# Kernel tuning notes

Hardware: AMD Instinct MI355X
Metric: run time of the kernel (lower is better)

Reference implementation:

```python
import jax, jax.numpy as jnp
import numpy as np
from jax import lax

B, S, HDIM = 4, 2048, 1024
H, D, L = 16, 64, 128
NB = S // L
EPS = 1e-8


def setup_inputs() -> dict:
    key = jax.random.key(0)
    ks = jax.random.split(key, 16)
    std = 0.02
    inp = {
        'f_in': jax.random.normal(ks[0], (B, S, HDIM), jnp.float32),
        'i_in': jax.random.normal(ks[1], (B, S, HDIM), jnp.float32),
        'z_in': jax.random.normal(ks[2], (B, S, HDIM), jnp.float32),
        'o_in': jax.random.normal(ks[3], (B, S, HDIM), jnp.float32),
        'c0': jax.random.normal(ks[4], (B, H, D), jnp.float32),
        'h0': jax.random.normal(ks[5], (B, H, D), jnp.float32),
        # weights stored (in, out) so forward is x @ W + b
        'Wf': std * jax.random.normal(ks[6], (HDIM, H * D), jnp.float32),
        'bf': jnp.zeros((H * D,), jnp.float32),
        'Wi': std * jax.random.normal(ks[7], (HDIM, H * D), jnp.float32),
        'bi': jnp.zeros((H * D,), jnp.float32),
        'Wz': std * jax.random.normal(ks[8], (HDIM, H * D), jnp.float32),
        'bz': jnp.zeros((H * D,), jnp.float32),
        'Wo': std * jax.random.normal(ks[9], (HDIM, H * D), jnp.float32),
        'bo': jnp.zeros((H * D,), jnp.float32),
        'Wp': std * jax.random.normal(ks[10], (H * D, HDIM), jnp.float32),
        'bp': jnp.zeros((HDIM,), jnp.float32),
    }
    return inp


def _to_blocks(x):
    # (B,S,H*D) -> (NB, B, H, D, L), matching torch view+permute(1,0,3,4,2)
    return jnp.transpose(x.reshape(B, NB, L, H, D), (1, 0, 3, 4, 2))


def _qlstm(f_in, i_in, z_in, o_in, c0, Wf, bf, Wi, bi, Wz, bz, Wo, bo, Wp, bp):
    fx = _to_blocks(f_in @ Wf + bf)
    ix = _to_blocks(i_in @ Wi + bi)
    zx = _to_blocks(z_in @ Wz + bz)
    ox = _to_blocks(o_in @ Wo + bo)

    f = jax.nn.sigmoid(fx + 1.0)              # (NB,B,H,D,L)
    o = jax.nn.sigmoid(ox)
    update = jax.nn.sigmoid(ix) * jnp.tanh(zx)

    kk = jnp.arange(L)[:, None]
    ll = jnp.arange(L + 1)[None, :]
    ones_mask = ll >= kk + 1                   # (L, L+1): filled with 1.0
    zeros_mask = ll >= kk + 2                  # (L, L+1): zeroed out

    def block_step(c, blk):
        fb, ob, ub = blk                       # each (B,H,D,L)
        cf = jnp.concatenate([fb, jnp.ones(fb.shape[:-1] + (1,), fb.dtype)], axis=-1)  # (B,H,D,L+1)
        Fm = jnp.broadcast_to(cf[..., None, :], fb.shape[:-1] + (L, L + 1))
        Fm = jnp.where(ones_mask, 1.0, Fm)
        # reversed log-cumsum-exp along last axis (decay products)
        Fm = jnp.exp(jnp.flip(jnp.cumsum(jnp.flip(jnp.log(Fm + EPS), -1), -1), -1)) - EPS
        Fm = jnp.where(zeros_mask, 0.0, Fm)    # (B,H,D,L,L+1)
        u = jnp.concatenate([c[..., None], ub], axis=-1)   # (B,H,D,L+1)
        cs = jnp.einsum('bhdkl,bhdl->bhdk', Fm, u)          # (B,H,D,L)
        hs = ob * jnp.tanh(cs)
        return cs[..., -1], hs

    last_c, hs = lax.scan(block_step, c0, (f, o, update))   # hs: (NB,B,H,D,L)
    last_h = hs[-1, ..., -1]
    y = jnp.transpose(hs, (1, 0, 4, 2, 3)).reshape(B, S, H * D)
    y = y @ Wp + bp                            # (B,S,HDIM)
    return y, last_c, last_h


def reference(f_in, i_in, z_in, o_in, c0, h0, Wf, bf, Wi, bi, Wz, bz, Wo, bo, Wp, bp):
    y, last_c, last_h = _qlstm(f_in, i_in, z_in, o_in, c0,
                               Wf, bf, Wi, bi, Wz, bz, Wo, bo, Wp, bp)
    return y, last_c, last_h
```

## Files before the change

kernel.cpp:

```cpp
#include <hip/hip_runtime.h>
#include <hip/hip_bf16.h>
#include <stdint.h>

constexpr int GM = 8192;
constexpr int GK = 1024;
constexpr int GN = 1024;
constexpr size_t NACT = (size_t)GM * GN;
constexpr int CHUNK = 32;
constexpr int NCHUNK = 64;
constexpr int NCH = 4096;
constexpr int NT = GK / 64;

#define DEVINL __device__ __forceinline__

typedef __attribute__((ext_vector_type(8))) short bf16x8;
typedef __attribute__((ext_vector_type(4))) float f32x4;

DEVINL float sigmoidf_(float x) { return 1.0f / (1.0f + __expf(-x)); }

DEVINL unsigned short f2bf(float x) {
  unsigned int u = __builtin_bit_cast(unsigned int, x);
  unsigned int rnd = 0x7fffu + ((u >> 16) & 1u);
  return (unsigned short)((u + rnd) >> 16);
}
DEVINL float bf2f(unsigned short u) {
  unsigned int x = ((unsigned int)u) << 16;
  return __builtin_bit_cast(float, x);
}

DEVINL void gload16(const void* g, void* l) {
  __builtin_amdgcn_global_load_lds(
      (const __attribute__((address_space(1))) unsigned int*)g,
      (__attribute__((address_space(3))) unsigned int*)l, 16, 0, 0);
}

#define SB() __builtin_amdgcn_sched_barrier(0)

struct PrepArgs {
  const float* csrc[4];
  unsigned short* cdst[4];
  const float* tsrc[5];
  unsigned short* tdst[5];
};

__global__ __launch_bounds__(256) void prep_kernel(PrepArgs p) {
  const int bx = blockIdx.x;
  if (bx < 4096) {
    const float* s = p.csrc[bx >> 10];
    unsigned short* d = p.cdst[bx >> 10];
    int i = (bx & 1023) * 256 + threadIdx.x;
    const int stride = 1024 * 256;
#pragma unroll
    for (int it = 0; it < 8; ++it, i += stride) {
      float4 v = ((const float4*)s)[i];
      ushort4 o;
      o.x = f2bf(v.x); o.y = f2bf(v.y); o.z = f2bf(v.z); o.w = f2bf(v.w);
      ((ushort4*)d)[i] = o;
    }
  } else {
    const int t = bx - 4096;
    const float* __restrict__ W = p.tsrc[t >> 10];
    unsigned short* __restrict__ Wt = p.tdst[t >> 10];
    const int rem = t & 1023;
    const int n0 = (rem & 31) * 32, k0 = (rem >> 5) * 32;
    __shared__ float tile[32][33];
    int tx = threadIdx.x & 31, ty = threadIdx.x >> 5;
#pragma unroll
    for (int i = 0; i < 32; i += 8)
      tile[ty + i][tx] = W[(size_t)(k0 + ty + i) * GN + n0 + tx];
    __syncthreads();
#pragma unroll
    for (int i = 0; i < 32; i += 8)
      Wt[(size_t)(n0 + ty + i) * GK + k0 + tx] = f2bf(tile[tx][ty + i]);
  }
}

DEVINL void gemm256_core(const unsigned short* __restrict__ A,
                         const unsigned short* __restrict__ W,
                         char* lds, int tid, int wave, int lane,
                         int bm, int bn, f32x4 (&acc)[8][4]) {
  const int Ah = wave >> 2;
  const int wn = (wave & 3) * 64;
  const int lrow = lane & 15;
  const int lgrp = lane >> 4;

  const char* gsrc[8];
  char* ldst[8];
  {
    const char* Ag = (const char*)A;
    const char* Wg = (const char*)W;
#pragma unroll
    for (int hh = 0; hh < 4; ++hh)
#pragma unroll
      for (int j = 0; j < 2; ++j) {
        const int lbyte = j * 8192 + tid * 16;
        const int row = lbyte >> 7;
        const int gcb = (lbyte & 127) ^ ((row & 7) << 4);
        const int i = hh * 2 + j;
        gsrc[i] = (hh < 2)
            ? Ag + (size_t)(bm * 256 + hh * 128 + row) * 2048 + gcb
            : Wg + (size_t)(bn * 256 + (hh - 2) * 128 + row) * 2048 + gcb;
        ldst[i] = lds + (hh >= 2 ? 32768 : 0) + (hh & 1) * 16384 + j * 8192 +
                  wave * 1024;
      }
  }

#pragma unroll
  for (int i = 0; i < 8; ++i) gload16(gsrc[i], ldst[i]);

  bf16x8 aF[4][2], bF[4][2];

  for (int t = 0; t < NT; ++t) {
    const int cur = t & 1;
    const int obuf = (cur ^ 1) * 65536;
    const char* Abase = lds + cur * 65536 + Ah * 16384;
    const char* Bbase = lds + cur * 65536 + 32768;
    const int nk = (t + 1 < NT) ? (t + 1) : (NT - 1);
    const size_t koff = (size_t)nk * 128;

#pragma unroll
    for (int i = 0; i < 4; ++i) gload16(gsrc[i] + koff, ldst[i] + obuf);
    asm volatile("s_waitcnt vmcnt(4)" ::: "memory");
    __builtin_amdgcn_s_barrier();
    SB();
#pragma unroll
    for (int m = 0; m < 4; ++m)
#pragma unroll
      for (int ks = 0; ks < 2; ++ks) {
        const int r = m * 16 + lrow;
        const int cb = ks * 64 + lgrp * 16;
        aF[m][ks] = *(const bf16x8*)(Abase + r * 128 + (cb ^ ((r & 7) << 4)));
      }
#pragma unroll
    for (int n = 0; n < 2; ++n)
#pragma unroll
      for (int ks = 0; ks < 2; ++ks) {
        const int nr = wn + n * 16 + lrow;
        const int cb = ks * 64 + lgrp * 16;
        bF[n][ks] = *(const bf16x8*)(Bbase + nr * 128 + (cb ^ ((nr & 7) << 4)));
      }
    __builtin_amdgcn_s_setprio(1);
#pragma unroll
    for (int m = 0; m < 4; ++m)
#pragma unroll
      for (int n = 0; n < 2; ++n)
#pragma unroll
        for (int ks = 0; ks < 2; ++ks)
          acc[m][n] = __builtin_amdgcn_mfma_f32_16x16x32_bf16(aF[m][ks], bF[n][ks],
                                                              acc[m][n], 0, 0, 0);
    __builtin_amdgcn_s_setprio(0);

#pragma unroll
    for (int n = 2; n < 4; ++n)
#pragma unroll
      for (int ks = 0; ks < 2; ++ks) {
        const int nr = wn + n * 16 + lrow;
        const int cb = ks * 64 + lgrp * 16;
        bF[n][ks] = *(const bf16x8*)(Bbase + nr * 128 + (cb ^ ((nr & 7) << 4)));
      }
#pragma unroll
    for (int i = 4; i < 8; ++i) gload16(gsrc[i] + koff, ldst[i] + obuf);
    __builtin_amdgcn_s_barrier();
    asm volatile("s_waitcnt lgkmcnt(0)" ::: "memory");
    SB();
    __builtin_amdgcn_s_setprio(1);
#pragma unroll
    for (int m = 0; m < 4; ++m)
#pragma unroll
      for (int n = 2; n < 4; ++n)
#pragma unroll
        for (int ks = 0; ks < 2; ++ks)
          acc[m][n] = __builtin_amdgcn_mfma_f32_16x16x32_bf16(aF[m][ks], bF[n][ks],
                                                              acc[m][n], 0, 0, 0);
    __builtin_amdgcn_s_setprio(0);

#pragma unroll
    for (int m = 0; m < 4; ++m)
#pragma unroll
      for (int ks = 0; ks < 2; ++ks) {
        const int r = (m + 4) * 16 + lrow;
        const int cb = ks * 64 + lgrp * 16;
        aF[m][ks] = *(const bf16x8*)(Abase + r * 128 + (cb ^ ((r & 7) << 4)));
      }
    __builtin_amdgcn_s_barrier();
    asm volatile("s_waitcnt lgkmcnt(0)" ::: "memory");
    SB();
    __builtin_amdgcn_s_setprio(1);
#pragma unroll
    for (int m = 0; m < 4; ++m)
#pragma unroll
      for (int n = 2; n < 4; ++n)
#pragma unroll
        for (int ks = 0; ks < 2; ++ks)
          acc[m + 4][n] = __builtin_amdgcn_mfma_f32_16x16x32_bf16(aF[m][ks], bF[n][ks],
                                                                  acc[m + 4][n], 0, 0, 0);
    __builtin_amdgcn_s_setprio(0);

    __builtin_amdgcn_s_setprio(1);
#pragma unroll
    for (int m = 0; m < 4; ++m)
#pragma unroll
      for (int n = 0; n < 2; ++n)
#pragma unroll
        for (int ks = 0; ks < 2; ++ks)
          acc[m + 4][n] = __builtin_amdgcn_mfma_f32_16x16x32_bf16(aF[m][ks], bF[n][ks],
                                                                  acc[m + 4][n], 0, 0, 0);
    __builtin_amdgcn_s_setprio(0);
  }
}

struct GateArgs {
  const unsigned short* A[4];
  const unsigned short* W[4];
  const float* bias[4];
  unsigned short* out[4];
};

__global__ __launch_bounds__(512, 2) void gemm_gates8(GateArgs ga) {
  extern __shared__ char lds[];
  const int tid = threadIdx.x;
  const int wave = tid >> 6, lane = tid & 63;
  const int bm = blockIdx.x, bn = blockIdx.y, gz = blockIdx.z;
  const int wm = (wave >> 2) * 128, wn = (wave & 3) * 64;
  const int lrow = lane & 15, lgrp = lane >> 4;

  f32x4 acc[8][4];
#pragma unroll
  for (int m = 0; m < 8; ++m)
#pragma unroll
    for (int n = 0; n < 4; ++n) acc[m][n] = (f32x4){0.f, 0.f, 0.f, 0.f};

  gemm256_core(ga.A[gz], ga.W[gz], lds, tid, wave, lane, bm, bn, acc);

  const float* bias = ga.bias[gz];
  unsigned short* out = ga.out[gz];
  float bv[4];
#pragma unroll
  for (int n = 0; n < 4; ++n) bv[n] = bias[bn * 256 + wn + n * 16 + lrow];

#pragma unroll
  for (int m = 0; m < 8; ++m)
#pragma unroll
    for (int n = 0; n < 4; ++n) {
      const int gc = bn * 256 + wn + n * 16 + lrow;
#pragma unroll
      for (int j = 0; j < 4; ++j) {
        const int gr = bm * 256 + wm + m * 16 + lgrp * 4 + j;
        float v = acc[m][n][j] + bv[n];
        if (gz == 0) v = sigmoidf_(v + 1.0f);
        else if (gz == 1) v = sigmoidf_(v);
        out[(size_t)gr * GN + gc] = f2bf(v);
      }
    }
}

__global__ __launch_bounds__(512, 2) void gemm_proj_bn128(
    const unsigned short* __restrict__ A, const unsigned short* __restrict__ W,
    const float* __restrict__ bias, float* __restrict__ out) {
  extern __shared__ char lds[];
  const int tid = threadIdx.x;
  const int wave = tid >> 6, lane = tid & 63;
  const int bm = blockIdx.x, bn = blockIdx.y;
  const int wm = (wave >> 2) * 128, wn = (wave & 3) * 32;
  const int lrow = lane & 15, lgrp = lane >> 4;

  f32x4 acc[8][2];
#pragma unroll
  for (int m = 0; m < 8; ++m)
#pragma unroll
    for (int n = 0; n < 2; ++n) acc[m][n] = (f32x4){0.f, 0.f, 0.f, 0.f};

  const char* gsrc[6];
  char* ldst[6];
  {
    const char* Ag = (const char*)A;
    const char* Wg = (const char*)W;
#pragma unroll
    for (int i = 0; i < 4; ++i) {
      const int lbyte = i * 8192 + tid * 16;
      const int row = lbyte >> 7;
      const int gcb = (lbyte & 127) ^ ((row & 7) << 4);
      gsrc[i] = Ag + (size_t)(bm * 256 + row) * 2048 + gcb;
      ldst[i] = lds + i * 8192 + wave * 1024;
    }
#pragma unroll
    for (int j = 0; j < 2; ++j) {
      const int lbyte = j * 8192 + tid * 16;
      const int row = lbyte >> 7;
      const int gcb = (lbyte & 127) ^ ((row & 7) << 4);
      gsrc[4 + j] = Wg + (size_t)(bn * 128 + row) * 2048 + gcb;
      ldst[4 + j] = lds + 65536 + j * 8192 + wave * 1024;
    }
  }

#pragma unroll
  for (int i = 0; i < 6; ++i) gload16(gsrc[i], ldst[i]);

  bf16x8 aLo[4][2], aHi[4][2], bF[2][2];

  for (int t = 0; t < NT; ++t) {
    const int cur = t & 1;
    const int obufA = (cur ^ 1) * 32768;
    const int obufB = (cur ^ 1) * 16384;
    const char* Abase = lds + cur * 32768;
    const char* Bbase = lds + 65536 + cur * 16384;
    const int nk = (t + 1 < NT) ? (t + 1) : (NT - 1);
    const size_t koff = (size_t)nk * 128;

#pragma unroll
    for (int i = 0; i < 4; ++i) gload16(gsrc[i] + koff, ldst[i] + obufA);
    asm volatile("s_waitcnt vmcnt(4)" ::: "memory");
    __builtin_amdgcn_s_barrier();
    SB();
#pragma unroll
    for (int m = 0; m < 4; ++m)
#pragma unroll
      for (int ks = 0; ks < 2; ++ks) {
        const int r = wm + m * 16 + lrow;
        const int cb = ks * 64 + lgrp * 16;
        aLo[m][ks] = *(const bf16x8*)(Abase + r * 128 + (cb ^ ((r & 7) << 4)));
      }
#pragma unroll
    for (int n = 0; n < 2; ++n)
#pragma unroll
      for (int ks = 0; ks < 2; ++ks) {
        const int nr = wn + n * 16 + lrow;
        const int cb = ks * 64 + lgrp * 16;
        bF[n][ks] = *(const bf16x8*)(Bbase + nr * 128 + (cb ^ ((nr & 7) << 4)));
      }
    __builtin_amdgcn_s_setprio(1);
#pragma unroll
    for (int m = 0; m < 4; ++m)
#pragma unroll
      for (int n = 0; n < 2; ++n)
#pragma unroll
        for (int ks = 0; ks < 2; ++ks)
          acc[m][n] = __builtin_amdgcn_mfma_f32_16x16x32_bf16(aLo[m][ks], bF[n][ks],
                                                              acc[m][n], 0, 0, 0);
    __builtin_amdgcn_s_setprio(0);

#pragma unroll
    for (int m = 0; m < 4; ++m)
#pragma unroll
      for (int ks = 0; ks < 2; ++ks) {
        const int r = wm + (m + 4) * 16 + lrow;
        const int cb = ks * 64 + lgrp * 16;
        aHi[m][ks] = *(const bf16x8*)(Abase + r * 128 + (cb ^ ((r & 7) << 4)));
      }
#pragma unroll
    for (int j = 4; j < 6; ++j) gload16(gsrc[j] + koff, ldst[j] + obufB);
    __builtin_amdgcn_s_barrier();
    asm volatile("s_waitcnt lgkmcnt(0)" ::: "memory");
    SB();
    __builtin_amdgcn_s_setprio(1);
#pragma unroll
    for (int m = 0; m < 4; ++m)
#pragma unroll
      for (int n = 0; n < 2; ++n)
#pragma unroll
        for (int ks = 0; ks < 2; ++ks)
          acc[m + 4][n] = __builtin_amdgcn_mfma_f32_16x16x32_bf16(aHi[m][ks], bF[n][ks],
                                                                  acc[m + 4][n], 0, 0, 0);
    __builtin_amdgcn_s_setprio(0);
  }

  float bv[2];
#pragma unroll
  for (int n = 0; n < 2; ++n) bv[n] = bias[bn * 128 + wn + n * 16 + lrow];

#pragma unroll
  for (int m = 0; m < 8; ++m)
#pragma unroll
    for (int n = 0; n < 2; ++n) {
      const int gc = bn * 128 + wn + n * 16 + lrow;
#pragma unroll
      for (int j = 0; j < 4; ++j) {
        const int gr = bm * 256 + wm + m * 16 + lgrp * 4 + j;
        out[(size_t)gr * GN + gc] = acc[m][n][j] + bv[n];
      }
    }
}

__global__ void scan_phaseA_kernel(const unsigned short* __restrict__ F,
                                   const unsigned short* __restrict__ Ip,
                                   const unsigned short* __restrict__ Zp,
                                   float* __restrict__ Pt, float* __restrict__ Ct) {
  int tid = blockIdx.x * blockDim.x + threadIdx.x;
  int ch = tid & (NCH - 1), chunk = tid >> 12;
  int b = ch >> 10, n = ch & 1023;
  size_t base = ((size_t)(b * 2048 + chunk * CHUNK)) * 1024 + n;
  float c = 0.f, P = 1.f;
#pragma unroll 8
  for (int t = 0; t < CHUNK; ++t) {
    size_t idx = base + (size_t)t * 1024;
    float f = bf2f(F[idx]);
    float u = sigmoidf_(bf2f(Ip[idx])) * tanhf(bf2f(Zp[idx]));
    c = __builtin_fmaf(f, c, u);
    P *= f;
  }
  Pt[tid] = P;
  Ct[tid] = c;
}

__global__ void scan_combine_kernel(const float* __restrict__ Pt,
                                    const float* __restrict__ Ct,
                                    const float* __restrict__ c0,
                                    float* __restrict__ Cin,
                                    float* __restrict__ last_c) {
  int ch = blockIdx.x * blockDim.x + threadIdx.x;
  float c = c0[ch];
#pragma unroll
  for (int j = 0; j < NCHUNK; ++j) {
    Cin[j * NCH + ch] = c;
    c = __builtin_fmaf(Pt[j * NCH + ch], c, Ct[j * NCH + ch]);
  }
  last_c[ch] = c;
}

__global__ void scan_phaseC_kernel(const unsigned short* __restrict__ F,
                                   const unsigned short* __restrict__ Ip,
                                   const unsigned short* __restrict__ Zp,
                                   const unsigned short* __restrict__ O,
                                   const float* __restrict__ Cin,
                                   unsigned short* __restrict__ Hb,
                                   float* __restrict__ last_h) {
  int tid = blockIdx.x * blockDim.x + threadIdx.x;
  int ch = tid & (NCH - 1), chunk = tid >> 12;
  int b = ch >> 10, n = ch & 1023;
  size_t base = ((size_t)(b * 2048 + chunk * CHUNK)) * 1024 + n;
  float c = Cin[tid];
  float h = 0.f;
#pragma unroll 8
  for (int t = 0; t < CHUNK; ++t) {
    size_t idx = base + (size_t)t * 1024;
    float f = bf2f(F[idx]);
    float u = sigmoidf_(bf2f(Ip[idx])) * tanhf(bf2f(Zp[idx]));
    float o = bf2f(O[idx]);
    c = __builtin_fmaf(f, c, u);
    h = o * tanhf(c);
    Hb[idx] = f2bf(h);
  }
  if (chunk == NCHUNK - 1) last_h[ch] = h;
}

extern "C" void kernel_launch(void* const* d_in, const int* in_sizes, int n_in,
                              void* d_out, int out_size, void* d_ws, size_t ws_size,
                              hipStream_t stream) {
  const float* f_in = (const float*)d_in[0];
  const float* i_in = (const float*)d_in[1];
  const float* z_in = (const float*)d_in[2];
  const float* o_in = (const float*)d_in[3];
  const float* c0 = (const float*)d_in[4];
  const float* Wf = (const float*)d_in[6];
  const float* bf_ = (const float*)d_in[7];
  const float* Wi = (const float*)d_in[8];
  const float* bi = (const float*)d_in[9];
  const float* Wz = (const float*)d_in[10];
  const float* bz = (const float*)d_in[11];
  const float* Wo = (const float*)d_in[12];
  const float* bo = (const float*)d_in[13];
  const float* Wp = (const float*)d_in[14];
  const float* bp = (const float*)d_in[15];

  float* y = (float*)d_out;
  float* last_c = y + NACT;
  float* last_h = last_c + NCH;

  char* w = (char*)d_ws;
  const size_t ABYTES = NACT * 2;
  const size_t WBYTES = (size_t)GK * GN * 2;
  unsigned short* Af = (unsigned short*)(w + 0 * ABYTES);
  unsigned short* Ai = (unsigned short*)(w + 1 * ABYTES);
  unsigned short* Az = (unsigned short*)(w + 2 * ABYTES);
  unsigned short* Ao = (unsigned short*)(w + 3 * ABYTES);
  char* wt = w + 4 * ABYTES;
  unsigned short* Wtf = (unsigned short*)(wt + 0 * WBYTES);
  unsigned short* Wti = (unsigned short*)(wt + 1 * WBYTES);
  unsigned short* Wtz = (unsigned short*)(wt + 2 * WBYTES);
  unsigned short* Wto = (unsigned short*)(wt + 3 * WBYTES);
  unsigned short* Wtp = (unsigned short*)(wt + 4 * WBYTES);
  char* gp = wt + 5 * WBYTES;
  unsigned short* F = (unsigned short*)(gp + 0 * ABYTES);
  unsigned short* O = (unsigned short*)(gp + 1 * ABYTES);
  unsigned short* Ip = (unsigned short*)(gp + 2 * ABYTES);
  unsigned short* Zp = (unsigned short*)(gp + 3 * ABYTES);
  unsigned short* Hb = Af;
  char* sp = gp + 4 * ABYTES;
  const size_t SBYTES = (size_t)NCH * NCHUNK * 4;
  float* Pt = (float*)(sp + 0 * SBYTES);
  float* Ct = (float*)(sp + 1 * SBYTES);
  float* Cin = (float*)(sp + 2 * SBYTES);

  (void)hipFuncSetAttribute((const void*)gemm_gates8,
                            hipFuncAttributeMaxDynamicSharedMemorySize, 131072);
  (void)hipFuncSetAttribute((const void*)gemm_proj_bn128,
                            hipFuncAttributeMaxDynamicSharedMemorySize, 98304);

  PrepArgs pa;
  pa.csrc[0] = f_in; pa.csrc[1] = o_in; pa.csrc[2] = i_in; pa.csrc[3] = z_in;
  pa.cdst[0] = Af;   pa.cdst[1] = Ao;   pa.cdst[2] = Ai;   pa.cdst[3] = Az;
  pa.tsrc[0] = Wf; pa.tsrc[1] = Wi; pa.tsrc[2] = Wz; pa.tsrc[3] = Wo; pa.tsrc[4] = Wp;
  pa.tdst[0] = Wtf; pa.tdst[1] = Wti; pa.tdst[2] = Wtz; pa.tdst[3] = Wto; pa.tdst[4] = Wtp;
  prep_kernel<<<9216, 256, 0, stream>>>(pa);

  GateArgs ga;
  ga.A[0] = Af;  ga.A[1] = Ao;  ga.A[2] = Ai;  ga.A[3] = Az;
  ga.W[0] = Wtf; ga.W[1] = Wto; ga.W[2] = Wti; ga.W[3] = Wtz;
  ga.bias[0] = bf_; ga.bias[1] = bo; ga.bias[2] = bi; ga.bias[3] = bz;
  ga.out[0] = F; ga.out[1] = O; ga.out[2] = Ip; ga.out[3] = Zp;
  gemm_gates8<<<dim3(GM / 256, GN / 256, 4), 512, 131072, stream>>>(ga);

  scan_phaseA_kernel<<<(NCH * NCHUNK) / 256, 256, 0, stream>>>(F, Ip, Zp, Pt, Ct);
  scan_combine_kernel<<<NCH / 256, 256, 0, stream>>>(Pt, Ct, c0, Cin, last_c);
  scan_phaseC_kernel<<<(NCH * NCHUNK) / 256, 256, 0, stream>>>(F, Ip, Zp, O, Cin, Hb,
                                                               last_h);

  gemm_proj_bn128<<<dim3(GM / 256, GN / 128), 512, 98304, stream>>>(Hb, Wtp, bp, y);
}
```

Baseline: 199.4 us.

## Halve gate GEMM K-tile to 32 and use sigmoid-based tanh in scans

The gate GEMM now stages K-slices of 32 instead of 64, with a new XOR swizzle sized for 64-byte rows. This halves LDS use to 64KB and halves the fragment registers, and launch bounds now request 4 blocks per CU instead of 2 to gain occupancy. The trade-off is twice as many loop iterations and barriers per block. Separately, the scan kernels replace tanhf with a cheaper 2*sigmoid(2x)-1 form, which may slightly change numerical accuracy.

```diff
diff --git a/kernel.cpp b/kernel.cpp
--- a/kernel.cpp
+++ b/kernel.cpp
@@ -9,7 +9,8 @@
 constexpr int CHUNK = 32;
 constexpr int NCHUNK = 64;
 constexpr int NCH = 4096;
-constexpr int NT = GK / 64;
+constexpr int NT32 = GK / 32;
+constexpr int NT64 = GK / 64;
 
 #define DEVINL __device__ __forceinline__
 
@@ -17,6 +18,7 @@
 typedef __attribute__((ext_vector_type(4))) float f32x4;
 
 DEVINL float sigmoidf_(float x) { return 1.0f / (1.0f + __expf(-x)); }
+DEVINL float fast_tanh(float x) { return __builtin_fmaf(2.0f, sigmoidf_(2.0f * x), -1.0f); }
 
 DEVINL unsigned short f2bf(float x) {
   unsigned int u = __builtin_bit_cast(unsigned int, x);
@@ -35,6 +37,8 @@
 }
 
 #define SB() __builtin_amdgcn_sched_barrier(0)
+
+DEVINL int swz32(int r) { return (((r & 3) ^ ((r >> 2) & 3)) << 4); }
 
 struct PrepArgs {
   const float* csrc[4];
@@ -75,7 +79,7 @@
   }
 }
 
-DEVINL void gemm256_core(const unsigned short* __restrict__ A,
+DEVINL void gates_core32(const unsigned short* __restrict__ A,
                          const unsigned short* __restrict__ W,
                          char* lds, int tid, int wave, int lane,
                          int bm, int bn, f32x4 (&acc)[8][4]) {
@@ -83,83 +87,72 @@
   const int wn = (wave & 3) * 64;
   const int lrow = lane & 15;
   const int lgrp = lane >> 4;
-
-  const char* gsrc[8];
-  char* ldst[8];
+  const int cb = lgrp * 16;
+
+  const char* gsrc[4];
+  char* ldst[4];
   {
     const char* Ag = (const char*)A;
     const char* Wg = (const char*)W;
 #pragma unroll
-    for (int hh = 0; hh < 4; ++hh)
+    for (int op = 0; op < 2; ++op)
 #pragma unroll
       for (int j = 0; j < 2; ++j) {
         const int lbyte = j * 8192 + tid * 16;
-        const int row = lbyte >> 7;
-        const int gcb = (lbyte & 127) ^ ((row & 7) << 4);
-        const int i = hh * 2 + j;
-        gsrc[i] = (hh < 2)
-            ? Ag + (size_t)(bm * 256 + hh * 128 + row) * 2048 + gcb
-            : Wg + (size_t)(bn * 256 + (hh - 2) * 128 + row) * 2048 + gcb;
-        ldst[i] = lds + (hh >= 2 ? 32768 : 0) + (hh & 1) * 16384 + j * 8192 +
-                  wave * 1024;
+        const int row = lbyte >> 6;
+        const int gcb = (lbyte & 63) ^ swz32(row);
+        const int i = op * 2 + j;
+        gsrc[i] = (op == 0)
+            ? Ag + (size_t)(bm * 256 + row) * 2048 + gcb
+            : Wg + (size_t)(bn * 256 + row) * 2048 + gcb;
+        ldst[i] = lds + op * 16384 + j * 8192 + wave * 1024;
       }
   }
 
 #pragma unroll
-  for (int i = 0; i < 8; ++i) gload16(gsrc[i], ldst[i]);
-
-  bf16x8 aF[4][2], bF[4][2];
-
-  for (int t = 0; t < NT; ++t) {
+  for (int i = 0; i < 4; ++i) gload16(gsrc[i], ldst[i]);
+
+  bf16x8 aF[4], bF[4];
+
+  for (int t = 0; t < NT32; ++t) {
     const int cur = t & 1;
-    const int obuf = (cur ^ 1) * 65536;
-    const char* Abase = lds + cur * 65536 + Ah * 16384;
-    const char* Bbase = lds + cur * 65536 + 32768;
-    const int nk = (t + 1 < NT) ? (t + 1) : (NT - 1);
-    const size_t koff = (size_t)nk * 128;
-
-#pragma unroll
-    for (int i = 0; i < 4; ++i) gload16(gsrc[i] + koff, ldst[i] + obuf);
-    asm volatile("s_waitcnt vmcnt(4)" ::: "memory");
+    const int obuf = (cur ^ 1) * 32768;
+    const char* Abase = lds + cur * 32768 + Ah * 8192;
+    const char* Bbase = lds + cur * 32768 + 16384;
+    const int nk = (t + 1 < NT32) ? (t + 1) : (NT32 - 1);
+    const size_t koff = (size_t)nk * 64;
+
+#pragma unroll
+    for (int i = 0; i < 2; ++i) gload16(gsrc[i] + koff, ldst[i] + obuf);
+    asm volatile("s_waitcnt vmcnt(2)" ::: "memory");
     __builtin_amdgcn_s_barrier();
     SB();
 #pragma unroll
-    for (int m = 0; m < 4; ++m)
-#pragma unroll
-      for (int ks = 0; ks < 2; ++ks) {
-        const int r = m * 16 + lrow;
-        const int cb = ks * 64 + lgrp * 16;
-        aF[m][ks] = *(const bf16x8*)(Abase + r * 128 + (cb ^ ((r & 7) << 4)));
-      }
-#pragma unroll
-    for (int n = 0; n < 2; ++n)
-#pragma unroll
-      for (int ks = 0; ks < 2; ++ks) {
-        const int nr = wn + n * 16 + lrow;
-        const int cb = ks * 64 + lgrp * 16;
-        bF[n][ks] = *(const bf16x8*)(Bbase + nr * 128 + (cb ^ ((nr & 7) << 4)));
-      }
+    for (int m = 0; m < 4; ++m) {
+      const int r = m * 16 + lrow;
+      aF[m] = *(const bf16x8*)(Abase + r * 64 + (cb ^ swz32(r)));
+    }
+#pragma unroll
+    for (int n = 0; n < 2; ++n) {
+      const int nr = wn + n * 16 + lrow;
+      bF[n] = *(const bf16x8*)(Bbase + nr * 64 + (cb ^ swz32(nr)));
+    }
     __builtin_amdgcn_s_setprio(1);
 #pragma unroll
     for (int m = 0; m < 4; ++m)
 #pragma unroll
       for (int n = 0; n < 2; ++n)
-#pragma unroll
-        for (int ks = 0; ks < 2; ++ks)
-          acc[m][n] = __builtin_amdgcn_mfma_f32_16x16x32_bf16(aF[m][ks], bF[n][ks],
-                                                              acc[m][n], 0, 0, 0);
+        acc[m][n] = __builtin_amdgcn_mfma_f32_16x16x32_bf16(aF[m], bF[n],
+                                                            acc[m][n], 0, 0, 0);
     __builtin_amdgcn_s_setprio(0);
 
 #pragma unroll
-    for (int n = 2; n < 4; ++n)
-#pragma unroll
-      for (int ks = 0; ks < 2; ++ks) {
-        const int nr = wn + n * 16 + lrow;
-        const int cb = ks * 64 + lgrp * 16;
-        bF[n][ks] = *(const bf16x8*)(Bbase + nr * 128 + (cb ^ ((nr & 7) << 4)));
-      }
-#pragma unroll
-    for (int i = 4; i < 8; ++i) gload16(gsrc[i] + koff, ldst[i] + obuf);
+    for (int n = 2; n < 4; ++n) {
+      const int nr = wn + n * 16 + lrow;
+      bF[n] = *(const bf16x8*)(Bbase + nr * 64 + (cb ^ swz32(nr)));
+    }
+#pragma unroll
+    for (int i = 2; i < 4; ++i) gload16(gsrc[i] + koff, ldst[i] + obuf);
     __builtin_amdgcn_s_barrier();
     asm volatile("s_waitcnt lgkmcnt(0)" ::: "memory");
     SB();
@@ -168,20 +161,15 @@
     for (int m = 0; m < 4; ++m)
 #pragma unroll
       for (int n = 2; n < 4; ++n)
-#pragma unroll
-        for (int ks = 0; ks < 2; ++ks)
-          acc[m][n] = __builtin_amdgcn_mfma_f32_16x16x32_bf16(aF[m][ks], bF[n][ks],
-                                                              acc[m][n], 0, 0, 0);
+        acc[m][n] = __builtin_amdgcn_mfma_f32_16x16x32_bf16(aF[m], bF[n],
+                                                            acc[m][n], 0, 0, 0);
     __builtin_amdgcn_s_setprio(0);
 
 #pragma unroll
-    for (int m = 0; m < 4; ++m)
-#pragma unroll
-      for (int ks = 0; ks < 2; ++ks) {
-        const int r = (m + 4) * 16 + lrow;
-        const int cb = ks * 64 + lgrp * 16;
-        aF[m][ks] = *(const bf16x8*)(Abase + r * 128 + (cb ^ ((r & 7) << 4)));
-      }
+    for (int m = 0; m < 4; ++m) {
+      const int r = (m + 4) * 16 + lrow;
+      aF[m] = *(const bf16x8*)(Abase + r * 64 + (cb ^ swz32(r)));
+    }
     __builtin_amdgcn_s_barrier();
     asm volatile("s_waitcnt lgkmcnt(0)" ::: "memory");
     SB();
@@ -190,10 +178,8 @@
     for (int m = 0; m < 4; ++m)
 #pragma unroll
       for (int n = 2; n < 4; ++n)
-#pragma unroll
-        for (int ks = 0; ks < 2; ++ks)
-          acc[m + 4][n] = __builtin_amdgcn_mfma_f32_16x16x32_bf16(aF[m][ks], bF[n][ks],
-                                                                  acc[m + 4][n], 0, 0, 0);
+        acc[m + 4][n] = __builtin_amdgcn_mfma_f32_16x16x32_bf16(aF[m], bF[n],
+                                                                acc[m + 4][n], 0, 0, 0);
     __builtin_amdgcn_s_setprio(0);
 
     __builtin_amdgcn_s_setprio(1);
@@ -201,10 +187,8 @@
     for (int m = 0; m < 4; ++m)
 #pragma unroll
       for (int n = 0; n < 2; ++n)
-#pragma unroll
-        for (int ks = 0; ks < 2; ++ks)
-          acc[m + 4][n] = __builtin_amdgcn_mfma_f32_16x16x32_bf16(aF[m][ks], bF[n][ks],
-                                                                  acc[m + 4][n], 0, 0, 0);
+        acc[m + 4][n] = __builtin_amdgcn_mfma_f32_16x16x32_bf16(aF[m], bF[n],
+                                                                acc[m + 4][n], 0, 0, 0);
     __builtin_amdgcn_s_setprio(0);
   }
 }
@@ -216,7 +200,7 @@
   unsigned short* out[4];
 };
 
-__global__ __launch_bounds__(512, 2) void gemm_gates8(GateArgs ga) {
+__global__ __launch_bounds__(512, 4) void gemm_gates8(GateArgs ga) {
   extern __shared__ char lds[];
   const int tid = threadIdx.x;
   const int wave = tid >> 6, lane = tid & 63;
@@ -230,7 +214,7 @@
 #pragma unroll
     for (int n = 0; n < 4; ++n) acc[m][n] = (f32x4){0.f, 0.f, 0.f, 0.f};
 
-  gemm256_core(ga.A[gz], ga.W[gz], lds, tid, wave, lane, bm, bn, acc);
+  gates_core32(ga.A[gz], ga.W[gz], lds, tid, wave, lane, bm, bn, acc);
 
   const float* bias = ga.bias[gz];
   unsigned short* out = ga.out[gz];
@@ -298,13 +282,13 @@
 
   bf16x8 aLo[4][2], aHi[4][2], bF[2][2];
 
-  for (int t = 0; t < NT; ++t) {
+  for (int t = 0; t < NT64; ++t) {
     const int cur = t & 1;
     const int obufA = (cur ^ 1) * 32768;
     const int obufB = (cur ^ 1) * 16384;
     const char* Abase = lds + cur * 32768;
     const char* Bbase = lds + 65536 + cur * 16384;
-    const int nk = (t + 1 < NT) ? (t + 1) : (NT - 1);
+    const int nk = (t + 1 < NT64) ? (t + 1) : (NT64 - 1);
     const size_t koff = (size_t)nk * 128;
 
 #pragma unroll
@@ -394,7 +378,7 @@
   for (int t = 0; t < CHUNK; ++t) {
     size_t idx = base + (size_t)t * 1024;
     float f = bf2f(F[idx]);
-    float u = sigmoidf_(bf2f(Ip[idx])) * tanhf(bf2f(Zp[idx]));
+    float u = sigmoidf_(bf2f(Ip[idx])) * fast_tanh(bf2f(Zp[idx]));
     c = __builtin_fmaf(f, c, u);
     P *= f;
   }
@@ -434,10 +418,10 @@
   for (int t = 0; t < CHUNK; ++t) {
     size_t idx = base + (size_t)t * 1024;
     float f = bf2f(F[idx]);
-    float u = sigmoidf_(bf2f(Ip[idx])) * tanhf(bf2f(Zp[idx]));
+    float u = sigmoidf_(bf2f(Ip[idx])) * fast_tanh(bf2f(Zp[idx]));
     float o = bf2f(O[idx]);
     c = __builtin_fmaf(f, c, u);
-    h = o * tanhf(c);
+    h = o * fast_tanh(c);
     Hb[idx] = f2bf(h);
   }
   if (chunk == NCHUNK - 1) last_h[ch] = h;
@@ -492,7 +476,7 @@
   float* Cin = (float*)(sp + 2 * SBYTES);
 
   (void)hipFuncSetAttribute((const void*)gemm_gates8,
-                            hipFuncAttributeMaxDynamicSharedMemorySize, 131072);
+                            hipFuncAttributeMaxDynamicSharedMemorySize, 65536);
   (void)hipFuncSetAttribute((const void*)gemm_proj_bn128,
                             hipFuncAttributeMaxDynamicSharedMemorySize, 98304);
 
@@ -508,7 +492,7 @@
   ga.W[0] = Wtf; ga.W[1] = Wto; ga.W[2] = Wti; ga.W[3] = Wtz;
   ga.bias[0] = bf_; ga.bias[1] = bo; ga.bias[2] = bi; ga.bias[3] = bz;
   ga.out[0] = F; ga.out[1] = O; ga.out[2] = Ip; ga.out[3] = Zp;
-  gemm_gates8<<<dim3(GM / 256, GN / 256, 4), 512, 131072, stream>>>(ga);
+  gemm_gates8<<<dim3(GM / 256, GN / 256, 4), 512, 65536, stream>>>(ga);
 
   scan_phaseA_kernel<<<(NCH * NCHUNK) / 256, 256, 0, stream>>>(F, Ip, Zp, Pt, Ct);
   scan_combine_kernel<<<NCH / 256, 256, 0, stream>>>(Pt, Ct, c0, Cin, last_c);
```

New measurement: 669.6 us. 236% more time.
